# Kernel tuning notes

Measured on AMD Instinct MI355X. Metric: run time of the kernel, lower is better.

The kernel has to match this reference:

```python
import jax, jax.numpy as jnp
import numpy as np

D_MODEL = 1024
N_HEADS = 16
HEAD_DIM = D_MODEL // N_HEADS
B, S = 4, 2048


def setup_inputs() -> dict:
    key = jax.random.key(0)
    ks = jax.random.split(key, 12)
    scale = 1.0 / np.sqrt(D_MODEL)
    inp = {
        "query": jax.random.normal(ks[0], (B, S, D_MODEL), dtype=jnp.float32),
        "key": jax.random.normal(ks[1], (B, S, D_MODEL), dtype=jnp.float32),
        "value": jax.random.normal(ks[2], (B, S, D_MODEL), dtype=jnp.float32),
        "mask": jnp.ones((B, 1, S), dtype=jnp.int32),
        "Wq": jax.random.normal(ks[3], (D_MODEL, D_MODEL), dtype=jnp.float32) * scale,
        "bq": jnp.zeros((D_MODEL,), dtype=jnp.float32),
        "Wk": jax.random.normal(ks[4], (D_MODEL, D_MODEL), dtype=jnp.float32) * scale,
        "bk": jnp.zeros((D_MODEL,), dtype=jnp.float32),
        "Wv": jax.random.normal(ks[5], (D_MODEL, D_MODEL), dtype=jnp.float32) * scale,
        "bv": jnp.zeros((D_MODEL,), dtype=jnp.float32),
        "Wo": jax.random.normal(ks[6], (D_MODEL, D_MODEL), dtype=jnp.float32) * scale,
        "bo": jnp.zeros((D_MODEL,), dtype=jnp.float32),
    }
    return inp


def reference(query, key, value, mask, Wq, bq, Wk, bk, Wv, bv, Wo, bo):
    bsz = query.shape[0]
    # Linear projections (torch nn.Linear: x @ W.T + b), split into heads -> [b, h, s, d]
    def proj(x, W, b):
        y = jnp.einsum("bse,de->bsd", x, W) + b
        return y.reshape(bsz, -1, N_HEADS, HEAD_DIM).transpose(0, 2, 1, 3)

    q = proj(query, Wq, bq)
    k = proj(key, Wk, bk)
    v = proj(value, Wv, bv)

    # NOTE: faithful to source — scale by 1/sqrt(d_model), not 1/sqrt(head_dim)
    scores = jnp.einsum("bhqd,bhkd->bhqk", q, k) / jnp.sqrt(jnp.asarray(D_MODEL, q.dtype))
    # mask [b, 1, s_k] -> unsqueeze(1) -> [b, 1, 1, s_k]; fill -inf where mask == 0
    m = mask[:, None, :, :]
    scores = jnp.where(m == 0, jnp.asarray(-jnp.inf, scores.dtype), scores)
    p_attn = jax.nn.softmax(scores, axis=-1)
    ctx = jnp.einsum("bhqk,bhkd->bhqd", p_attn, v)

    concat = ctx.transpose(0, 2, 1, 3).reshape(bsz, -1, D_MODEL)
    out = jnp.einsum("bse,de->bsd", concat, Wo) + bo
    return out
```

## Files before the change

kernel.cpp:

```cpp
#include <hip/hip_runtime.h>
#include <hip/hip_bf16.h>

typedef unsigned short u16;
typedef __attribute__((ext_vector_type(4))) short short4v;
typedef __attribute__((ext_vector_type(8))) short short8;
typedef __attribute__((ext_vector_type(4))) float float4v;
typedef __attribute__((ext_vector_type(16))) float f32x16;

__device__ __forceinline__ void async_copy16(const void* g, void* l) {
  __builtin_amdgcn_global_load_lds(
      (const __attribute__((address_space(1))) unsigned int*)g,
      (__attribute__((address_space(3))) unsigned int*)l,
      16, 0, 0);
}

__device__ __forceinline__ u16 f2bf(float f) {
  __hip_bfloat16 h = __float2bfloat16(f);
  return *reinterpret_cast<u16*>(&h);
}

__device__ __forceinline__ unsigned pack2(float a, float b) {
  return (unsigned)f2bf(a) | ((unsigned)f2bf(b) << 16);
}

__device__ __forceinline__ float exp2_fast(float x) {
  return __builtin_amdgcn_exp2f(x);
}

struct CArgs {
  const float* in[7];
  u16* out[7];
  int n[7];
};

__global__ void conv_bf16(CArgs a) {
  int t = blockIdx.y;
  int n = a.n[t];
  long i = ((long)blockIdx.x * blockDim.x + threadIdx.x) * 8;
  if (i >= n) return;
  const float4v* f = (const float4v*)(a.in[t] + i);
  float4v lo = f[0], hi = f[1];
  u16 o[8];
  o[0] = f2bf(lo.x); o[1] = f2bf(lo.y); o[2] = f2bf(lo.z); o[3] = f2bf(lo.w);
  o[4] = f2bf(hi.x); o[5] = f2bf(hi.y); o[6] = f2bf(hi.z); o[7] = f2bf(hi.w);
  *(short8*)(a.out[t] + i) = *(const short8*)o;
}

template <bool OUT_F32>
__device__ __forceinline__
void gemm_body(const u16* __restrict__ A, const u16* __restrict__ W,
               const float* __restrict__ bias, void* __restrict__ Cp,
               int M, int N, int K, int mode) {
  __shared__ __attribute__((aligned(16))) u16 As[128 * 32];
  __shared__ __attribute__((aligned(16))) u16 Ws[128 * 32];

  const int tid  = threadIdx.x;
  const int lane = tid & 63;
  const int wave = tid >> 6;
  const int ln15 = lane & 15;
  const int quad = lane >> 4;

  int bx = blockIdx.x, by = blockIdx.y;
  {
    const int nwg = gridDim.x * gridDim.y;
    if (gridDim.x == 8 && (nwg & 7) == 0) {
      const int per = nwg >> 3;
      const int bid = by * 8 + bx;
      const int nlin = (bid & 7) * per + (bid >> 3);
      bx = nlin & 7;
      by = nlin >> 3;
    }
  }
  const int m0 = by * 128;
  const int n0 = bx * 128;
  const int wm = (wave & 1) * 64;
  const int wn = (wave >> 1) * 64;

  float4v acc[4][4];
#pragma unroll
  for (int i = 0; i < 4; i++)
#pragma unroll
    for (int j = 0; j < 4; j++) acc[i][j] = (float4v)0.0f;

  for (int k0 = 0; k0 < K; k0 += 32) {
#pragma unroll
    for (int c = 0; c < 2; c++) {
      int e = (c * 256 + tid) * 8;
      int r = e >> 5, col = e & 31;
      async_copy16(A + (size_t)(m0 + r) * K + k0 + col, (void*)(As + e));
      async_copy16(W + (size_t)(n0 + r) * K + k0 + col, (void*)(Ws + e));
    }
    __syncthreads();

    short8 af[4], bfr[4];
#pragma unroll
    for (int i = 0; i < 4; i++)
      af[i] = *(const short8*)(As + (wm + i * 16 + ln15) * 32 + quad * 8);
#pragma unroll
    for (int j = 0; j < 4; j++)
      bfr[j] = *(const short8*)(Ws + (wn + j * 16 + ln15) * 32 + quad * 8);
#pragma unroll
    for (int i = 0; i < 4; i++)
#pragma unroll
      for (int j = 0; j < 4; j++)
        acc[i][j] = __builtin_amdgcn_mfma_f32_16x16x32_bf16(af[i], bfr[j], acc[i][j], 0, 0, 0);
    __syncthreads();
  }

#pragma unroll
  for (int j = 0; j < 4; j++) {
    int n = n0 + wn + j * 16 + ln15;
    float bval = bias[n];
#pragma unroll
    for (int i = 0; i < 4; i++) {
#pragma unroll
      for (int r = 0; r < 4; r++) {
        int m = m0 + wm + i * 16 + quad * 4 + r;
        float v = acc[i][j][r] + bval;
        size_t addr;
        if (mode == 0) {
          addr = (size_t)m * N + n;
        } else {
          int b = m >> 11, s = m & 2047;
          int h = n >> 6, dh = n & 63;
          if (mode == 1) addr = (((size_t)(b * 16 + h)) * 2048 + s) * 64 + dh;
          else           addr = (((size_t)(b * 16 + h)) * 64 + dh) * 2048 + s;
        }
        if (OUT_F32) ((float*)Cp)[addr] = v;
        else         ((u16*)Cp)[addr] = f2bf(v);
      }
    }
  }
}

template <bool OUT_F32>
__global__ __launch_bounds__(256, 3)
void gemm_bt(const u16* __restrict__ A, const u16* __restrict__ W,
             const float* __restrict__ bias, void* __restrict__ Cp,
             int M, int N, int K, int mode) {
  gemm_body<OUT_F32>(A, W, bias, Cp, M, N, K, mode);
}

struct G3 {
  const u16* A[3]; const u16* W[3]; const float* bias[3];
  void* C[3]; int mode[3];
};

__global__ __launch_bounds__(256, 3)
void gemm_qkv(G3 g) {
  const int z = blockIdx.z;
  gemm_body<false>(g.A[z], g.W[z], g.bias[z], g.C[z], 8192, 1024, 1024, g.mode[z]);
}

#define SWZ(c, r) ((c) ^ (((r) & 7) << 3))
__global__ __launch_bounds__(256, 4)
void attn(const u16* __restrict__ Q, const u16* __restrict__ K,
          const u16* __restrict__ Vt, const int* __restrict__ mask,
          u16* __restrict__ Ct) {
  __shared__ __attribute__((aligned(16))) u16 Ks[2][64 * 64];
  __shared__ __attribute__((aligned(16))) u16 Vs[2][64 * 64];

  const int tid  = threadIdx.x;
  const int lane = tid & 63;
  const int wave = tid >> 6;
  const int ln31 = lane & 31;
  const int hi   = lane >> 5;
  const int bh = blockIdx.y;
  const int b = bh >> 4, h = bh & 15;
  const int q0 = blockIdx.x * 128;
  const int qr0 = wave * 32;

  const u16* Qg = Q + ((size_t)bh * 2048 + q0 + qr0) * 64;
  const u16* Kg = K + (size_t)bh * 2048 * 64;
  const u16* Vg = Vt + (size_t)bh * 64 * 2048;
  const int* mg = mask + b * 2048;

  const float C2 = 0.04508422f;


  short8 qf[4];
#pragma unroll
  for (int m = 0; m < 4; m++)
    qf[m] = *(const short8*)(Qg + (size_t)ln31 * 64 + m * 16 + hi * 8);

#pragma unroll
  for (int c = 0; c < 2; c++) {
    int e = (c * 256 + tid) * 8;
    int r = e >> 6, col = e & 63;
    int scol = SWZ(col, r);
    async_copy16(Kg + (size_t)r * 64 + scol, (void*)(Ks[0] + e));
    async_copy16(Vg + (size_t)r * 2048 + scol, (void*)(Vs[0] + e));
  }

  f32x16 acc[2];
#pragma unroll
  for (int d = 0; d < 2; d++) acc[d] = (f32x16)0.0f;
  float lrow = 0.0f;

  for (int t = 0; t < 32; t++) {
    const int buf = t & 1;
    __syncthreads();

    if ((t + 1) < 32) {
      const int kt2 = (t + 1) * 64;
#pragma unroll
      for (int c = 0; c < 2; c++) {
        int e = (c * 256 + tid) * 8;
        int r = e >> 6, col = e & 63;
        int scol = SWZ(col, r);
        async_copy16(Kg + (size_t)(kt2 + r) * 64 + scol, (void*)(Ks[buf ^ 1] + e));
        async_copy16(Vg + (size_t)r * 2048 + kt2 + scol, (void*)(Vs[buf ^ 1] + e));
      }
    }

    unsigned bw[2][2][4];
#pragma unroll
    for (int kb = 0; kb < 2; kb++) {
      f32x16 s = (f32x16)0.0f;
      __builtin_amdgcn_s_setprio(1);
#pragma unroll
      for (int m = 0; m < 4; m++) {
        const int krow = kb * 32 + ln31;
        short8 kf = *(const short8*)(Ks[buf] + krow * 64 + SWZ(m * 16 + hi * 8, krow));
        s = __builtin_amdgcn_mfma_f32_32x32x16_bf16(kf, qf[m], s, 0, 0, 0);
      }
      __builtin_amdgcn_s_setprio(0);
      unsigned w[8];
#pragma unroll
      for (int g = 0; g < 4; g++) {
        int4 m4 = *(const int4*)(mg + t * 64 + kb * 32 + g * 8 + hi * 4);
        float mb0 = (m4.x == 0) ? -1.5e30f : 0.0f;
        float mb1 = (m4.y == 0) ? -1.5e30f : 0.0f;
        float mb2 = (m4.z == 0) ? -1.5e30f : 0.0f;
        float mb3 = (m4.w == 0) ? -1.5e30f : 0.0f;
        float p0 = exp2_fast(fmaf(s[4 * g + 0], C2, mb0));
        float p1 = exp2_fast(fmaf(s[4 * g + 1], C2, mb1));
        float p2 = exp2_fast(fmaf(s[4 * g + 2], C2, mb2));
        float p3 = exp2_fast(fmaf(s[4 * g + 3], C2, mb3));
        lrow += (p0 + p1) + (p2 + p3);
        w[2 * g]     = pack2(p0, p1);
        w[2 * g + 1] = pack2(p2, p3);
      }
#pragma unroll
      for (int c = 0; c < 2; c++) {
        auto r0 = __builtin_amdgcn_permlane32_swap(w[c], w[2 + c], false, false);
        bw[kb][0][c]     = r0[0];
        bw[kb][0][2 + c] = r0[1];
        auto r1 = __builtin_amdgcn_permlane32_swap(w[4 + c], w[6 + c], false, false);
        bw[kb][1][c]     = r1[0];
        bw[kb][1][2 + c] = r1[1];
      }
    }

    __builtin_amdgcn_s_setprio(1);
#pragma unroll
    for (int d = 0; d < 2; d++) {
#pragma unroll
      for (int kb = 0; kb < 2; kb++) {
#pragma unroll
        for (int mp = 0; mp < 2; mp++) {
          const int vrow = d * 32 + ln31;
          short8 vf = *(const short8*)(Vs[buf] + vrow * 64 +
                                       SWZ(kb * 32 + mp * 16 + hi * 8, vrow));
          union { unsigned w4[4]; short8 s8; } u;
          u.w4[0] = bw[kb][mp][0]; u.w4[1] = bw[kb][mp][1];
          u.w4[2] = bw[kb][mp][2]; u.w4[3] = bw[kb][mp][3];
          acc[d] = __builtin_amdgcn_mfma_f32_32x32x16_bf16(vf, u.s8, acc[d], 0, 0, 0);
        }
      }
    }
    __builtin_amdgcn_s_setprio(0);
  }

  float l = lrow + __shfl_xor(lrow, 32);
  float inv = 1.0f / l;
  const int s = q0 + qr0 + ln31;
  u16* base = Ct + ((size_t)(b * 2048 + s)) * 1024 + h * 64 + hi * 4;
#pragma unroll
  for (int d = 0; d < 2; d++) {
#pragma unroll
    for (int g = 0; g < 4; g++) {
      u16 o[4];
      o[0] = f2bf(acc[d][4 * g + 0] * inv);
      o[1] = f2bf(acc[d][4 * g + 1] * inv);
      o[2] = f2bf(acc[d][4 * g + 2] * inv);
      o[3] = f2bf(acc[d][4 * g + 3] * inv);
      *(short4v*)(base + d * 32 + g * 8) = *(const short4v*)o;
    }
  }
}


extern "C" void kernel_launch(void* const* d_in, const int* in_sizes, int n_in,
                              void* d_out, int out_size, void* d_ws, size_t ws_size,
                              hipStream_t stream) {
  int iq, ik, iv, im, iWq, ibq, iWk, ibk, iWv, ibv, iWo, ibo;
  if (in_sizes[0] == 8388608) {
    iq = 0; ik = 1; iv = 2; im = 3;
    iWq = 4; ibq = 5; iWk = 6; ibk = 7; iWv = 8; ibv = 9; iWo = 10; ibo = 11;
  } else {
    iWk = 0; iWo = 1; iWq = 2; iWv = 3;
    ibk = 4; ibo = 5; ibq = 6; ibv = 7;
    ik = 8; im = 9; iq = 10; iv = 11;
  }
  const float* query = (const float*)d_in[iq];
  const float* key   = (const float*)d_in[ik];
  const float* value = (const float*)d_in[iv];
  const int*   mask  = (const int*)d_in[im];
  const float* Wq = (const float*)d_in[iWq];
  const float* bq = (const float*)d_in[ibq];
  const float* Wk = (const float*)d_in[iWk];
  const float* bk = (const float*)d_in[ibk];
  const float* Wv = (const float*)d_in[iWv];
  const float* bv = (const float*)d_in[ibv];
  const float* Wo = (const float*)d_in[iWo];
  const float* bo = (const float*)d_in[ibo];

  const long U  = 8388608;
  const long Wn = 1048576;
  u16* ws = (u16*)d_ws;
  u16* cq   = ws;
  u16* ck   = cq + U;
  u16* cv   = ck + U;
  u16* cWq  = cv + U;
  u16* cWk  = cWq + Wn;
  u16* cWv  = cWk + Wn;
  u16* cWo  = cWv + Wn;
  u16* qws  = cWo + Wn;
  u16* kws  = qws + U;
  u16* cws  = ck;

  const size_t need_batched = (size_t)(7 * U + 4 * Wn) * sizeof(u16);
  const bool batched = ws_size >= need_batched;
  u16* vtws = batched ? (kws + U) : cq;

  dim3 blk(256);

  CArgs ca;
  ca.in[0] = query; ca.out[0] = cq;  ca.n[0] = (int)U;
  ca.in[1] = key;   ca.out[1] = ck;  ca.n[1] = (int)U;
  ca.in[2] = value; ca.out[2] = cv;  ca.n[2] = (int)U;
  ca.in[3] = Wq;    ca.out[3] = cWq; ca.n[3] = (int)Wn;
  ca.in[4] = Wk;    ca.out[4] = cWk; ca.n[4] = (int)Wn;
  ca.in[5] = Wv;    ca.out[5] = cWv; ca.n[5] = (int)Wn;
  ca.in[6] = Wo;    ca.out[6] = cWo; ca.n[6] = (int)Wn;
  conv_bf16<<<dim3(4096, 7), blk, 0, stream>>>(ca);

  dim3 gproj(8, 64);
  if (batched) {
    G3 g3;
    g3.A[0] = cq; g3.W[0] = cWq; g3.bias[0] = bq; g3.C[0] = qws;  g3.mode[0] = 1;
    g3.A[1] = ck; g3.W[1] = cWk; g3.bias[1] = bk; g3.C[1] = kws;  g3.mode[1] = 1;
    g3.A[2] = cv; g3.W[2] = cWv; g3.bias[2] = bv; g3.C[2] = vtws; g3.mode[2] = 2;
    gemm_qkv<<<dim3(8, 64, 3), blk, 0, stream>>>(g3);
  } else {
    gemm_bt<false><<<gproj, blk, 0, stream>>>(cq, cWq, bq, qws, 8192, 1024, 1024, 1);
    gemm_bt<false><<<gproj, blk, 0, stream>>>(ck, cWk, bk, kws, 8192, 1024, 1024, 1);
    gemm_bt<false><<<gproj, blk, 0, stream>>>(cv, cWv, bv, vtws, 8192, 1024, 1024, 2);
  }
  attn<<<dim3(16, 64), blk, 0, stream>>>(qws, kws, vtws, mask, cws);
  gemm_bt<true><<<gproj, blk, 0, stream>>>(cws, cWo, bo, d_out, 8192, 1024, 1024, 0);
}
```

Before: 390.7 us.

## Deepen GEMM K-tile with swizzled LDS, fold softmax scale into Q, skip mask when all-ones

```diff
diff --git a/kernel.cpp b/kernel.cpp
--- a/kernel.cpp
+++ b/kernel.cpp
@@ -6,6 +6,8 @@
 typedef __attribute__((ext_vector_type(8))) short short8;
 typedef __attribute__((ext_vector_type(4))) float float4v;
 typedef __attribute__((ext_vector_type(16))) float f32x16;
+
+#define SWZ(c, r) ((c) ^ (((r) & 7) << 3))
 
 __device__ __forceinline__ void async_copy16(const void* g, void* l) {
   __builtin_amdgcn_global_load_lds(
@@ -50,9 +52,9 @@
 __device__ __forceinline__
 void gemm_body(const u16* __restrict__ A, const u16* __restrict__ W,
                const float* __restrict__ bias, void* __restrict__ Cp,
-               int M, int N, int K, int mode) {
-  __shared__ __attribute__((aligned(16))) u16 As[128 * 32];
-  __shared__ __attribute__((aligned(16))) u16 Ws[128 * 32];
+               int M, int N, int K, int mode, float oscale) {
+  __shared__ __attribute__((aligned(16))) u16 As[128 * 64];
+  __shared__ __attribute__((aligned(16))) u16 Ws[128 * 64];
 
   const int tid  = threadIdx.x;
   const int lane = tid & 63;
@@ -82,28 +84,36 @@
 #pragma unroll
     for (int j = 0; j < 4; j++) acc[i][j] = (float4v)0.0f;
 
-  for (int k0 = 0; k0 < K; k0 += 32) {
-#pragma unroll
-    for (int c = 0; c < 2; c++) {
+  for (int k0 = 0; k0 < K; k0 += 64) {
+#pragma unroll
+    for (int c = 0; c < 4; c++) {
       int e = (c * 256 + tid) * 8;
-      int r = e >> 5, col = e & 31;
-      async_copy16(A + (size_t)(m0 + r) * K + k0 + col, (void*)(As + e));
-      async_copy16(W + (size_t)(n0 + r) * K + k0 + col, (void*)(Ws + e));
+      int r = e >> 6, col = e & 63;
+      int scol = SWZ(col, r);
+      async_copy16(A + (size_t)(m0 + r) * K + k0 + scol, (void*)(As + e));
+      async_copy16(W + (size_t)(n0 + r) * K + k0 + scol, (void*)(Ws + e));
     }
     __syncthreads();
 
-    short8 af[4], bfr[4];
-#pragma unroll
-    for (int i = 0; i < 4; i++)
-      af[i] = *(const short8*)(As + (wm + i * 16 + ln15) * 32 + quad * 8);
-#pragma unroll
-    for (int j = 0; j < 4; j++)
-      bfr[j] = *(const short8*)(Ws + (wn + j * 16 + ln15) * 32 + quad * 8);
-#pragma unroll
-    for (int i = 0; i < 4; i++)
-#pragma unroll
-      for (int j = 0; j < 4; j++)
-        acc[i][j] = __builtin_amdgcn_mfma_f32_16x16x32_bf16(af[i], bfr[j], acc[i][j], 0, 0, 0);
+#pragma unroll
+    for (int kk = 0; kk < 64; kk += 32) {
+      short8 af[4], bfr[4];
+#pragma unroll
+      for (int i = 0; i < 4; i++) {
+        const int row = wm + i * 16 + ln15;
+        af[i] = *(const short8*)(As + row * 64 + SWZ(kk + quad * 8, row));
+      }
+#pragma unroll
+      for (int j = 0; j < 4; j++) {
+        const int row = wn + j * 16 + ln15;
+        bfr[j] = *(const short8*)(Ws + row * 64 + SWZ(kk + quad * 8, row));
+      }
+#pragma unroll
+      for (int i = 0; i < 4; i++)
+#pragma unroll
+        for (int j = 0; j < 4; j++)
+          acc[i][j] = __builtin_amdgcn_mfma_f32_16x16x32_bf16(af[i], bfr[j], acc[i][j], 0, 0, 0);
+    }
     __syncthreads();
   }
 
@@ -116,7 +126,7 @@
 #pragma unroll
       for (int r = 0; r < 4; r++) {
         int m = m0 + wm + i * 16 + quad * 4 + r;
-        float v = acc[i][j][r] + bval;
+        float v = (acc[i][j][r] + bval) * oscale;
         size_t addr;
         if (mode == 0) {
           addr = (size_t)m * N + n;
@@ -137,22 +147,22 @@
 __global__ __launch_bounds__(256, 3)
 void gemm_bt(const u16* __restrict__ A, const u16* __restrict__ W,
              const float* __restrict__ bias, void* __restrict__ Cp,
-             int M, int N, int K, int mode) {
-  gemm_body<OUT_F32>(A, W, bias, Cp, M, N, K, mode);
+             int M, int N, int K, int mode, float oscale) {
+  gemm_body<OUT_F32>(A, W, bias, Cp, M, N, K, mode, oscale);
 }
 
 struct G3 {
   const u16* A[3]; const u16* W[3]; const float* bias[3];
-  void* C[3]; int mode[3];
+  void* C[3]; int mode[3]; float oscale[3];
 };
 
 __global__ __launch_bounds__(256, 3)
 void gemm_qkv(G3 g) {
   const int z = blockIdx.z;
-  gemm_body<false>(g.A[z], g.W[z], g.bias[z], g.C[z], 8192, 1024, 1024, g.mode[z]);
-}
-
-#define SWZ(c, r) ((c) ^ (((r) & 7) << 3))
+  gemm_body<false>(g.A[z], g.W[z], g.bias[z], g.C[z], 8192, 1024, 1024,
+                   g.mode[z], g.oscale[z]);
+}
+
 __global__ __launch_bounds__(256, 4)
 void attn(const u16* __restrict__ Q, const u16* __restrict__ K,
           const u16* __restrict__ Vt, const int* __restrict__ mask,
@@ -175,9 +185,6 @@
   const u16* Vg = Vt + (size_t)bh * 64 * 2048;
   const int* mg = mask + b * 2048;
 
-  const float C2 = 0.04508422f;
-
-
   short8 qf[4];
 #pragma unroll
   for (int m = 0; m < 4; m++)
@@ -213,6 +220,9 @@
       }
     }
 
+    const int mv = mg[t * 64 + lane];
+    const bool allone = (__ballot(mv != 0) == ~0ull);
+
     unsigned bw[2][2][4];
 #pragma unroll
     for (int kb = 0; kb < 2; kb++) {
@@ -226,20 +236,33 @@
       }
       __builtin_amdgcn_s_setprio(0);
       unsigned w[8];
-#pragma unroll
-      for (int g = 0; g < 4; g++) {
-        int4 m4 = *(const int4*)(mg + t * 64 + kb * 32 + g * 8 + hi * 4);
-        float mb0 = (m4.x == 0) ? -1.5e30f : 0.0f;
-        float mb1 = (m4.y == 0) ? -1.5e30f : 0.0f;
-        float mb2 = (m4.z == 0) ? -1.5e30f : 0.0f;
-        float mb3 = (m4.w == 0) ? -1.5e30f : 0.0f;
-        float p0 = exp2_fast(fmaf(s[4 * g + 0], C2, mb0));
-        float p1 = exp2_fast(fmaf(s[4 * g + 1], C2, mb1));
-        float p2 = exp2_fast(fmaf(s[4 * g + 2], C2, mb2));
-        float p3 = exp2_fast(fmaf(s[4 * g + 3], C2, mb3));
-        lrow += (p0 + p1) + (p2 + p3);
-        w[2 * g]     = pack2(p0, p1);
-        w[2 * g + 1] = pack2(p2, p3);
+      if (allone) {
+#pragma unroll
+        for (int g = 0; g < 4; g++) {
+          float p0 = exp2_fast(s[4 * g + 0]);
+          float p1 = exp2_fast(s[4 * g + 1]);
+          float p2 = exp2_fast(s[4 * g + 2]);
+          float p3 = exp2_fast(s[4 * g + 3]);
+          lrow += (p0 + p1) + (p2 + p3);
+          w[2 * g]     = pack2(p0, p1);
+          w[2 * g + 1] = pack2(p2, p3);
+        }
+      } else {
+#pragma unroll
+        for (int g = 0; g < 4; g++) {
+          int4 m4 = *(const int4*)(mg + t * 64 + kb * 32 + g * 8 + hi * 4);
+          float mb0 = (m4.x == 0) ? -1.5e30f : 0.0f;
+          float mb1 = (m4.y == 0) ? -1.5e30f : 0.0f;
+          float mb2 = (m4.z == 0) ? -1.5e30f : 0.0f;
+          float mb3 = (m4.w == 0) ? -1.5e30f : 0.0f;
+          float p0 = exp2_fast(s[4 * g + 0] + mb0);
+          float p1 = exp2_fast(s[4 * g + 1] + mb1);
+          float p2 = exp2_fast(s[4 * g + 2] + mb2);
+          float p3 = exp2_fast(s[4 * g + 3] + mb3);
+          lrow += (p0 + p1) + (p2 + p3);
+          w[2 * g]     = pack2(p0, p1);
+          w[2 * g + 1] = pack2(p2, p3);
+        }
       }
 #pragma unroll
       for (int c = 0; c < 2; c++) {
@@ -334,6 +357,8 @@
   const bool batched = ws_size >= need_batched;
   u16* vtws = batched ? (kws + U) : cq;
 
+  const float C2F = 0.04508422f;
+
   dim3 blk(256);
 
   CArgs ca;
@@ -349,15 +374,15 @@
   dim3 gproj(8, 64);
   if (batched) {
     G3 g3;
-    g3.A[0] = cq; g3.W[0] = cWq; g3.bias[0] = bq; g3.C[0] = qws;  g3.mode[0] = 1;
-    g3.A[1] = ck; g3.W[1] = cWk; g3.bias[1] = bk; g3.C[1] = kws;  g3.mode[1] = 1;
-    g3.A[2] = cv; g3.W[2] = cWv; g3.bias[2] = bv; g3.C[2] = vtws; g3.mode[2] = 2;
+    g3.A[0] = cq; g3.W[0] = cWq; g3.bias[0] = bq; g3.C[0] = qws;  g3.mode[0] = 1; g3.oscale[0] = C2F;
+    g3.A[1] = ck; g3.W[1] = cWk; g3.bias[1] = bk; g3.C[1] = kws;  g3.mode[1] = 1; g3.oscale[1] = 1.0f;
+    g3.A[2] = cv; g3.W[2] = cWv; g3.bias[2] = bv; g3.C[2] = vtws; g3.mode[2] = 2; g3.oscale[2] = 1.0f;
     gemm_qkv<<<dim3(8, 64, 3), blk, 0, stream>>>(g3);
   } else {
-    gemm_bt<false><<<gproj, blk, 0, stream>>>(cq, cWq, bq, qws, 8192, 1024, 1024, 1);
-    gemm_bt<false><<<gproj, blk, 0, stream>>>(ck, cWk, bk, kws, 8192, 1024, 1024, 1);
-    gemm_bt<false><<<gproj, blk, 0, stream>>>(cv, cWv, bv, vtws, 8192, 1024, 1024, 2);
+    gemm_bt<false><<<gproj, blk, 0, stream>>>(cq, cWq, bq, qws, 8192, 1024, 1024, 1, C2F);
+    gemm_bt<false><<<gproj, blk, 0, stream>>>(ck, cWk, bk, kws, 8192, 1024, 1024, 1, 1.0f);
+    gemm_bt<false><<<gproj, blk, 0, stream>>>(cv, cWv, bv, vtws, 8192, 1024, 1024, 2, 1.0f);
   }
   attn<<<dim3(16, 64), blk, 0, stream>>>(qws, kws, vtws, mask, cws);
-  gemm_bt<true><<<gproj, blk, 0, stream>>>(cws, cWo, bo, d_out, 8192, 1024, 1024, 0);
-}
+  gemm_bt<true><<<gproj, blk, 0, stream>>>(cws, cWo, bo, d_out, 8192, 1024, 1024, 0, 1.0f);
+}
```

Result: faster. 360.9 us (-7.6%).
